# Optimization experiments

Measured on AMD Instinct MI355X. Metric: run time of the kernel, lower is better.

## Reference

```python
import jax, jax.numpy as jnp
import numpy as np

EMBED = 2560
HEADS = 8
HEAD_DIM = EMBED // HEADS

def setup_inputs() -> dict:
    key = jax.random.key(0)
    k1, k2, k3, k4, k5 = jax.random.split(key, 5)
    x = jax.random.normal(k1, (2, 2048, EMBED), dtype=jnp.float32)
    # nn.Linear(embed, 3*embed): weight [3E, E], bias [3E]
    s = 1.0 / np.sqrt(EMBED)
    W_qkv = jax.random.uniform(k2, (3 * EMBED, EMBED), jnp.float32, -s, s)
    b_qkv = jax.random.uniform(k3, (3 * EMBED,), jnp.float32, -s, s)
    W_out = jax.random.uniform(k4, (EMBED, EMBED), jnp.float32, -s, s)
    b_out = jax.random.uniform(k5, (EMBED,), jnp.float32, -s, s)
    return {"x": x, "W_qkv": W_qkv, "b_qkv": b_qkv, "W_out": W_out, "b_out": b_out}

def reference(x, W_qkv, b_qkv, W_out, b_out):
    N, S, E = x.shape
    qkv = jnp.einsum('bse,fe->bsf', x, W_qkv) + b_qkv            # [B,S,3E]
    qkv = qkv.reshape(N, S, 3, HEADS, HEAD_DIM)
    q = jnp.transpose(qkv[:, :, 0], (0, 2, 1, 3))                 # [B,H,S,D]
    k = jnp.transpose(qkv[:, :, 1], (0, 2, 1, 3))
    v = jnp.transpose(qkv[:, :, 2], (0, 2, 1, 3))
    scale = jnp.sqrt(jnp.float32(HEAD_DIM))
    attn = jnp.einsum('bhqd,bhkd->bhqk', q, k) / scale            # [B,H,S,S]
    attn = jax.nn.softmax(attn, axis=-1)
    out = jnp.einsum('bhqk,bhkd->bhqd', attn, v)                  # [B,H,S,D]
    out = jnp.transpose(out, (0, 2, 1, 3)).reshape(N, S, E)
    return jnp.einsum('bse,fe->bsf', out, W_out) + b_out
```

## Files before the change

### kernel.cpp

```cpp
#include <hip/hip_runtime.h>

#define EMBED 2560
#define HEADS 8
#define HDIM  320
#define BATCH 2
#define SEQ   2048
#define MTOT  (BATCH*SEQ)
#define FTOT  (3*EMBED)

using bf = __bf16;
typedef __bf16 bf16x8 __attribute__((ext_vector_type(8)));
typedef float  f32x4  __attribute__((ext_vector_type(4)));
typedef short  s16x8  __attribute__((ext_vector_type(8)));
typedef float  f32x4v __attribute__((ext_vector_type(4)));

__device__ __forceinline__ void gl_lds16(const bf* g, bf* l) {
    __builtin_amdgcn_global_load_lds(
        (const __attribute__((address_space(1))) void*)g,
        (__attribute__((address_space(3))) void*)l,
        16, 0, 0);
}

__global__ void cvt_bf16(const float* __restrict__ in, bf* __restrict__ out, int n) {
    int i = (blockIdx.x*blockDim.x + threadIdx.x)*8;
    if (i >= n) return;
    f32x4v a = *reinterpret_cast<const f32x4v*>(in + i);
    f32x4v b = *reinterpret_cast<const f32x4v*>(in + i + 4);
    bf16x8 r;
    r[0]=(bf)a[0]; r[1]=(bf)a[1]; r[2]=(bf)a[2]; r[3]=(bf)a[3];
    r[4]=(bf)b[0]; r[5]=(bf)b[1]; r[6]=(bf)b[2]; r[7]=(bf)b[3];
    *reinterpret_cast<bf16x8*>(out + i) = r;
}

template<bool OUTBF>
__global__ void gemm_bt(const bf* __restrict__ A, const bf* __restrict__ B,
                        const float* __restrict__ bias, void* __restrict__ Cp,
                        int M, int N, int K) {
    __shared__ bf As[128*32];
    __shared__ bf Bs[128*32];
    const int tid = threadIdx.x, lane = tid & 63, wid = tid >> 6;
    const int wr = wid >> 1, wc = wid & 1;
    const int m0 = blockIdx.y*128, n0 = blockIdx.x*128;
    const int l15 = lane & 15, l4 = lane >> 4;
    f32x4 acc[4][4] = {};

    for (int k0 = 0; k0 < K; k0 += 32) {
        #pragma unroll
        for (int j = 0; j < 2; ++j) {
            int ch  = wid*128 + j*64 + lane;
            int row = ch >> 2, col = (ch & 3)*8;
            gl_lds16(A + (size_t)(m0 + row)*K + k0 + col, As + (wid*128 + j*64)*8);
            gl_lds16(B + (size_t)(n0 + row)*K + k0 + col, Bs + (wid*128 + j*64)*8);
        }
        __syncthreads();
        bf16x8 af[4], bfr[4];
        #pragma unroll
        for (int m = 0; m < 4; ++m)
            af[m] = *reinterpret_cast<const bf16x8*>(&As[(wr*64 + m*16 + l15)*32 + l4*8]);
        #pragma unroll
        for (int n = 0; n < 4; ++n)
            bfr[n] = *reinterpret_cast<const bf16x8*>(&Bs[(wc*64 + n*16 + l15)*32 + l4*8]);
        #pragma unroll
        for (int m = 0; m < 4; ++m)
            #pragma unroll
            for (int n = 0; n < 4; ++n)
                acc[m][n] = __builtin_amdgcn_mfma_f32_16x16x32_bf16(af[m], bfr[n], acc[m][n], 0, 0, 0);
        __syncthreads();
    }
    #pragma unroll
    for (int m = 0; m < 4; ++m) {
        #pragma unroll
        for (int n = 0; n < 4; ++n) {
            int col_g = n0 + wc*64 + n*16 + l15;
            float bv = bias[col_g];
            #pragma unroll
            for (int r = 0; r < 4; ++r) {
                int row_g = m0 + wr*64 + m*16 + l4*4 + r;
                float v = acc[m][n][r] + bv;
                if (OUTBF) ((bf*)Cp)[(size_t)row_g*N + col_g] = (bf)v;
                else       ((float*)Cp)[(size_t)row_g*N + col_g] = v;
            }
        }
    }
}

__global__ void repack_vt(const bf* __restrict__ qkv, bf* __restrict__ vt) {
    __shared__ bf tile[64][72];
    const int bh = blockIdx.z, b = bh >> 3, h = bh & 7;
    const int s0 = blockIdx.x*64, d0 = blockIdx.y*64;
    const int t = threadIdx.x;
    #pragma unroll
    for (int p = 0; p < 2; ++p) {
        int sr = (t >> 3) + p*32, ck = t & 7;
        s16x8 v = *reinterpret_cast<const s16x8*>(
            qkv + ((size_t)(b*SEQ + s0 + sr))*FTOT + 2*EMBED + h*HDIM + d0 + ck*8);
        *reinterpret_cast<s16x8*>(&tile[sr][ck*8]) = v;
    }
    __syncthreads();
    #pragma unroll
    for (int p = 0; p < 2; ++p) {
        int dr = (t >> 3) + p*32, ck = t & 7;
        bf16x8 r;
        #pragma unroll
        for (int j = 0; j < 8; ++j) r[j] = tile[ck*8 + j][dr];
        *reinterpret_cast<bf16x8*>(vt + ((size_t)bh*HDIM + d0 + dr)*SEQ + s0 + ck*8) = r;
    }
}

__global__ __launch_bounds__(512, 2)
void attn_fwd(const bf* __restrict__ qkv, const bf* __restrict__ vt, bf* __restrict__ aout) {
    __shared__ bf Kls[2][32*320];
    __shared__ bf Vls[2][320*32];
    __shared__ bf Ps[8][16][40];
    const int bh = blockIdx.y, b = bh >> 3, h = bh & 7;
    const int tid = threadIdx.x, lane = tid & 63, wid = tid >> 6;
    const int qw = blockIdx.x*128 + wid*16;
    const int l15 = lane & 15, l4 = lane >> 4;
    const float scale = 0.05590169944f;

    const bf* gsrc[5];
    int ldsoff[5];
    size_t step;
    if (wid < 4) {
        step = (size_t)32*FTOT;
        #pragma unroll
        for (int i = 0; i < 5; ++i) {
            int g = wid*5 + i;
            int q = g*64 + lane;
            int r = q/40, cl = q - r*40;
            int cg = cl ^ (r & 7);
            gsrc[i] = qkv + (size_t)(b*SEQ + r)*FTOT + EMBED + h*HDIM + cg*8;
            ldsoff[i] = g*512;
        }
    } else {
        step = 32;
        #pragma unroll
        for (int i = 0; i < 5; ++i) {
            int g = wid*5 + i - 20;
            int q = g*64 + lane;
            int row = q >> 2, cl = q & 3;
            int cg = cl ^ ((row >> 1) & 3);
            gsrc[i] = vt + (size_t)bh*HDIM*SEQ + (size_t)row*SEQ + cg*8;
            ldsoff[i] = g*512;
        }
    }

    bf16x8 qf[10];
    const bf* qbase = qkv + ((size_t)(b*SEQ + qw + l15))*FTOT + h*HDIM + l4*8;
    #pragma unroll
    for (int d = 0; d < 10; ++d) qf[d] = *reinterpret_cast<const bf16x8*>(qbase + d*32);

    f32x4 o[20] = {};
    float mrow[4], lsum[4];
    #pragma unroll
    for (int r = 0; r < 4; ++r) { mrow[r] = -1e30f; lsum[r] = 0.f; }

    const int r7  = l15 & 7;
    const int vsw = (l4 ^ ((l15 >> 1) & 3))*8;

    {
        bf* lb = (wid < 4) ? &Kls[0][0] : &Vls[0][0];
        #pragma unroll
        for (int i = 0; i < 5; ++i) { gl_lds16(gsrc[i], lb + ldsoff[i]); gsrc[i] += step; }
    }
    __syncthreads();

    for (int kt = 0; kt < SEQ/32; ++kt) {
        const int bb = kt & 1;
        if (kt + 1 < SEQ/32) {
            bf* lb = (wid < 4) ? &Kls[bb^1][0] : &Vls[bb^1][0];
            #pragma unroll
            for (int i = 0; i < 5; ++i) { gl_lds16(gsrc[i], lb + ldsoff[i]); gsrc[i] += step; }
        }
        const bf* Kb = &Kls[bb][0];
        const bf* Vb = &Vls[bb][0];

        f32x4 sc[2] = {};
        #pragma unroll
        for (int kb = 0; kb < 2; ++kb) {
            const int Rbase = (kb*16 + l15)*320;
            #pragma unroll
            for (int d = 0; d < 10; ++d) {
                int c = (d*4 + l4) ^ r7;
                bf16x8 kf = *reinterpret_cast<const bf16x8*>(&Kb[Rbase + c*8]);
                sc[kb] = __builtin_amdgcn_mfma_f32_16x16x32_bf16(qf[d], kf, sc[kb], 0, 0, 0);
            }
        }

        float tmax[4];
        bool need = false;
        #pragma unroll
        for (int r = 0; r < 4; ++r) {
            float v = fmaxf(sc[0][r], sc[1][r])*scale;
            v = fmaxf(v, __shfl_xor(v, 1));
            v = fmaxf(v, __shfl_xor(v, 2));
            v = fmaxf(v, __shfl_xor(v, 4));
            v = fmaxf(v, __shfl_xor(v, 8));
            tmax[r] = v;
            need = need || (v > mrow[r] + 8.f);
        }
        if (__any(need)) {
            float alpha[4];
            #pragma unroll
            for (int r = 0; r < 4; ++r) {
                float nm = fmaxf(mrow[r], tmax[r]);
                alpha[r] = __expf(mrow[r] - nm);
                mrow[r] = nm;
                lsum[r] *= alpha[r];
            }
            #pragma unroll
            for (int c = 0; c < 20; ++c)
                #pragma unroll
                for (int r = 0; r < 4; ++r) o[c][r] *= alpha[r];
        }

        float ps[2][4];
        #pragma unroll
        for (int r = 0; r < 4; ++r) {
            float p0 = __expf(sc[0][r]*scale - mrow[r]);
            float p1 = __expf(sc[1][r]*scale - mrow[r]);
            ps[0][r] = p0; ps[1][r] = p1;
            lsum[r] += p0 + p1;
        }

        #pragma unroll
        for (int kb = 0; kb < 2; ++kb)
            #pragma unroll
            for (int r = 0; r < 4; ++r)
                Ps[wid][l4*4 + r][kb*16 + l15] = (bf)ps[kb][r];

        bf16x8 pf = *reinterpret_cast<const bf16x8*>(&Ps[wid][l15][l4*8]);
        #pragma unroll
        for (int c = 0; c < 20; ++c) {
            bf16x8 vf = *reinterpret_cast<const bf16x8*>(&Vb[(c*16 + l15)*32 + vsw]);
            o[c] = __builtin_amdgcn_mfma_f32_16x16x32_bf16(pf, vf, o[c], 0, 0, 0);
        }
        __syncthreads();
    }

    float inv[4];
    #pragma unroll
    for (int r = 0; r < 4; ++r) {
        float s = lsum[r];
        s += __shfl_xor(s, 1);
        s += __shfl_xor(s, 2);
        s += __shfl_xor(s, 4);
        s += __shfl_xor(s, 8);
        inv[r] = 1.f/s;
    }
    #pragma unroll
    for (int c = 0; c < 20; ++c)
        #pragma unroll
        for (int r = 0; r < 4; ++r) {
            size_t idx = ((size_t)(b*SEQ + qw + l4*4 + r))*EMBED + h*HDIM + c*16 + l15;
            aout[idx] = (bf)(o[c][r]*inv[r]);
        }
}

extern "C" void kernel_launch(void* const* d_in, const int* in_sizes, int n_in,
                              void* d_out, int out_size, void* d_ws, size_t ws_size,
                              hipStream_t stream) {
    const float* x    = (const float*)d_in[0];
    const float* Wqkv = (const float*)d_in[1];
    const float* bqkv = (const float*)d_in[2];
    const float* Wout = (const float*)d_in[3];
    const float* bout = (const float*)d_in[4];
    float* out = (float*)d_out;

    char* ws = (char*)d_ws;
    bf* xb    = (bf*)(ws);
    bf* wqkvb = (bf*)(ws + 20971520);
    bf* woutb = (bf*)(ws + 60293120);
    bf* qkvb  = (bf*)(ws + 73400320);
    bf* vtb   = (bf*)(ws + 136314880);
    bf* attnb = xb;

    cvt_bf16<<<5120, 256, 0, stream>>>(x,    xb,    MTOT*EMBED);
    cvt_bf16<<<9600, 256, 0, stream>>>(Wqkv, wqkvb, FTOT*EMBED);
    cvt_bf16<<<3200, 256, 0, stream>>>(Wout, woutb, EMBED*EMBED);

    gemm_bt<true ><<<dim3(FTOT/128,  MTOT/128), 256, 0, stream>>>(xb, wqkvb, bqkv, qkvb, MTOT, FTOT, EMBED);
    repack_vt<<<dim3(SEQ/64, HDIM/64, BATCH*HEADS), 256, 0, stream>>>(qkvb, vtb);
    attn_fwd<<<dim3(SEQ/128, BATCH*HEADS), 512, 0, stream>>>(qkvb, vtb, attnb);
    gemm_bt<false><<<dim3(EMBED/128, MTOT/128), 256, 0, stream>>>(attnb, woutb, bout, out, MTOT, EMBED, EMBED);
}
```

Measured before the change: 492.2 us.

## Replace GEMM with 256x256 double-buffered swizzled LDS pipelined kernel

Swaps the simple 128x128, K=32 single-buffered GEMM for a 256x256-tile, K=64 kernel with 8 waves. It double-buffers A/B halves in LDS, XOR-swizzles the LDS layout to avoid bank conflicts, interleaves async global->LDS loads with MFMA phases under s_setprio, and remaps workgroup IDs so neighbouring blocks share data in cache. The goal is higher MFMA utilisation and fewer barrier stalls in both projection GEMMs. It uses much more LDS and many registers, and the out-projection grid shrinks to 160 blocks, which may leave CUs underused.

```diff
diff --git a/kernel.cpp b/kernel.cpp
--- a/kernel.cpp
+++ b/kernel.cpp
@@ -33,54 +33,166 @@
 }
 
 template<bool OUTBF>
-__global__ void gemm_bt(const bf* __restrict__ A, const bf* __restrict__ B,
-                        const float* __restrict__ bias, void* __restrict__ Cp,
-                        int M, int N, int K) {
-    __shared__ bf As[128*32];
-    __shared__ bf Bs[128*32];
+__global__ __launch_bounds__(512, 2)
+void gemm256(const bf* __restrict__ A, const bf* __restrict__ B,
+             const float* __restrict__ bias, void* __restrict__ Cp,
+             int M, int N, int K) {
+    __shared__ __align__(16) bf AsL[2][2][8192];
+    __shared__ __align__(16) bf BsL[2][2][8192];
     const int tid = threadIdx.x, lane = tid & 63, wid = tid >> 6;
-    const int wr = wid >> 1, wc = wid & 1;
-    const int m0 = blockIdx.y*128, n0 = blockIdx.x*128;
+    const int wr = wid >> 2, wc = wid & 3;
     const int l15 = lane & 15, l4 = lane >> 4;
-    f32x4 acc[4][4] = {};
-
-    for (int k0 = 0; k0 < K; k0 += 32) {
-        #pragma unroll
-        for (int j = 0; j < 2; ++j) {
-            int ch  = wid*128 + j*64 + lane;
-            int row = ch >> 2, col = (ch & 3)*8;
-            gl_lds16(A + (size_t)(m0 + row)*K + k0 + col, As + (wid*128 + j*64)*8);
-            gl_lds16(B + (size_t)(n0 + row)*K + k0 + col, Bs + (wid*128 + j*64)*8);
-        }
-        __syncthreads();
-        bf16x8 af[4], bfr[4];
-        #pragma unroll
-        for (int m = 0; m < 4; ++m)
-            af[m] = *reinterpret_cast<const bf16x8*>(&As[(wr*64 + m*16 + l15)*32 + l4*8]);
-        #pragma unroll
-        for (int n = 0; n < 4; ++n)
-            bfr[n] = *reinterpret_cast<const bf16x8*>(&Bs[(wc*64 + n*16 + l15)*32 + l4*8]);
-        #pragma unroll
-        for (int m = 0; m < 4; ++m)
-            #pragma unroll
-            for (int n = 0; n < 4; ++n)
-                acc[m][n] = __builtin_amdgcn_mfma_f32_16x16x32_bf16(af[m], bfr[n], acc[m][n], 0, 0, 0);
-        __syncthreads();
-    }
-    #pragma unroll
-    for (int m = 0; m < 4; ++m) {
-        #pragma unroll
-        for (int n = 0; n < 4; ++n) {
-            int col_g = n0 + wc*64 + n*16 + l15;
-            float bv = bias[col_g];
-            #pragma unroll
-            for (int r = 0; r < 4; ++r) {
-                int row_g = m0 + wr*64 + m*16 + l4*4 + r;
-                float v = acc[m][n][r] + bv;
-                if (OUTBF) ((bf*)Cp)[(size_t)row_g*N + col_g] = (bf)v;
-                else       ((float*)Cp)[(size_t)row_g*N + col_g] = v;
-            }
-        }
+
+    const int nwg = gridDim.x*gridDim.y;
+    int bid = blockIdx.y*gridDim.x + blockIdx.x;
+    if ((nwg & 7) == 0) bid = (bid & 7)*(nwg >> 3) + (bid >> 3);
+    const int m0 = (bid / gridDim.x)*256, n0 = (bid % gridDim.x)*256;
+    const int NT = K >> 6;
+
+    unsigned aOff[2];
+    #pragma unroll
+    for (int j = 0; j < 2; ++j) {
+        int q = (wid*2 + j)*64 + lane;
+        int r = q >> 3, cs = q & 7;
+        int csrc = ((((cs >> 1) ^ (r & 3)) << 1) | (cs & 1));
+        aOff[j] = (unsigned)r*K + csrc*8;
+    }
+    const bf* Ap = A + (size_t)m0*K;
+    const bf* Bp = B + (size_t)n0*K;
+
+    auto stA = [&](int bb, int h, int kt) {
+        bf* d = &AsL[bb][h][wid*1024];
+        const bf* s = Ap + (size_t)h*128*K + (size_t)kt*64;
+        gl_lds16(s + aOff[0], d);
+        gl_lds16(s + aOff[1], d + 512);
+    };
+    auto stB = [&](int bb, int h, int kt) {
+        bf* d = &BsL[bb][h][wid*1024];
+        const bf* s = Bp + (size_t)h*128*K + (size_t)kt*64;
+        gl_lds16(s + aOff[0], d);
+        gl_lds16(s + aOff[1], d + 512);
+    };
+
+    f32x4 acc[8][4] = {};
+    bf16x8 aR[4][2], bR0[2][2], bR1[2][2];
+
+    stB(0,0,0); stB(0,1,0); stA(0,0,0); stA(0,1,0); stB(1,0,1); stB(1,1,1);
+    asm volatile("s_waitcnt vmcnt(4)" ::: "memory");
+    __builtin_amdgcn_s_barrier();
+
+    const int brow0 = (wc & 1)*64;
+    for (int kt = 0; kt < NT; ++kt) {
+        const int bb = kt & 1;
+        const bf* Ab = &AsL[bb][wr][0];
+        const bf* Bb = &BsL[bb][wc >> 1][0];
+
+        #pragma unroll
+        for (int mi = 0; mi < 4; ++mi)
+            #pragma unroll
+            for (int kk = 0; kk < 2; ++kk) {
+                int r = mi*16 + l15;
+                int g = kk*2 + (l4 >> 1);
+                aR[mi][kk] = *reinterpret_cast<const bf16x8*>(&Ab[r*64 + ((g^(r&3))*16) + (l4&1)*8]);
+            }
+        #pragma unroll
+        for (int ni = 0; ni < 2; ++ni)
+            #pragma unroll
+            for (int kk = 0; kk < 2; ++kk) {
+                int r = brow0 + ni*16 + l15;
+                int g = kk*2 + (l4 >> 1);
+                bR0[ni][kk] = *reinterpret_cast<const bf16x8*>(&Bb[r*64 + ((g^(r&3))*16) + (l4&1)*8]);
+            }
+        if (kt + 1 < NT) stA(bb^1, 0, kt+1);
+        __builtin_amdgcn_s_barrier();
+        asm volatile("s_waitcnt lgkmcnt(0)" ::: "memory");
+        __builtin_amdgcn_sched_barrier(0);
+        __builtin_amdgcn_s_setprio(1);
+        #pragma unroll
+        for (int mi = 0; mi < 4; ++mi)
+            #pragma unroll
+            for (int ni = 0; ni < 2; ++ni)
+                #pragma unroll
+                for (int kk = 0; kk < 2; ++kk)
+                    acc[mi][ni] = __builtin_amdgcn_mfma_f32_16x16x32_bf16(aR[mi][kk], bR0[ni][kk], acc[mi][ni], 0, 0, 0);
+        __builtin_amdgcn_s_setprio(0);
+        __builtin_amdgcn_s_barrier();
+
+        #pragma unroll
+        for (int ni = 0; ni < 2; ++ni)
+            #pragma unroll
+            for (int kk = 0; kk < 2; ++kk) {
+                int r = brow0 + 32 + ni*16 + l15;
+                int g = kk*2 + (l4 >> 1);
+                bR1[ni][kk] = *reinterpret_cast<const bf16x8*>(&Bb[r*64 + ((g^(r&3))*16) + (l4&1)*8]);
+            }
+        if (kt + 1 < NT) stA(bb^1, 1, kt+1);
+        __builtin_amdgcn_s_barrier();
+        asm volatile("s_waitcnt lgkmcnt(0)" ::: "memory");
+        __builtin_amdgcn_sched_barrier(0);
+        __builtin_amdgcn_s_setprio(1);
+        #pragma unroll
+        for (int mi = 0; mi < 4; ++mi)
+            #pragma unroll
+            for (int ni = 0; ni < 2; ++ni)
+                #pragma unroll
+                for (int kk = 0; kk < 2; ++kk)
+                    acc[mi][2+ni] = __builtin_amdgcn_mfma_f32_16x16x32_bf16(aR[mi][kk], bR1[ni][kk], acc[mi][2+ni], 0, 0, 0);
+        __builtin_amdgcn_s_setprio(0);
+        __builtin_amdgcn_s_barrier();
+
+        #pragma unroll
+        for (int mi = 0; mi < 4; ++mi)
+            #pragma unroll
+            for (int kk = 0; kk < 2; ++kk) {
+                int r = 64 + mi*16 + l15;
+                int g = kk*2 + (l4 >> 1);
+                aR[mi][kk] = *reinterpret_cast<const bf16x8*>(&Ab[r*64 + ((g^(r&3))*16) + (l4&1)*8]);
+            }
+        if (kt + 2 < NT) stB(bb, 0, kt+2);
+        __builtin_amdgcn_s_barrier();
+        asm volatile("s_waitcnt lgkmcnt(0)" ::: "memory");
+        __builtin_amdgcn_sched_barrier(0);
+        __builtin_amdgcn_s_setprio(1);
+        #pragma unroll
+        for (int mi = 0; mi < 4; ++mi)
+            #pragma unroll
+            for (int ni = 0; ni < 2; ++ni)
+                #pragma unroll
+                for (int kk = 0; kk < 2; ++kk)
+                    acc[4+mi][2+ni] = __builtin_amdgcn_mfma_f32_16x16x32_bf16(aR[mi][kk], bR1[ni][kk], acc[4+mi][2+ni], 0, 0, 0);
+        __builtin_amdgcn_s_setprio(0);
+        __builtin_amdgcn_s_barrier();
+
+        if (kt + 2 < NT) stB(bb, 1, kt+2);
+        if (kt >= NT-2) asm volatile("s_waitcnt vmcnt(0)" ::: "memory");
+        else            asm volatile("s_waitcnt vmcnt(4)" ::: "memory");
+        __builtin_amdgcn_s_barrier();
+        __builtin_amdgcn_s_setprio(1);
+        #pragma unroll
+        for (int mi = 0; mi < 4; ++mi)
+            #pragma unroll
+            for (int ni = 0; ni < 2; ++ni)
+                #pragma unroll
+                for (int kk = 0; kk < 2; ++kk)
+                    acc[4+mi][ni] = __builtin_amdgcn_mfma_f32_16x16x32_bf16(aR[mi][kk], bR0[ni][kk], acc[4+mi][ni], 0, 0, 0);
+        __builtin_amdgcn_s_setprio(0);
+        __builtin_amdgcn_s_barrier();
+    }
+
+    const int cr0 = m0 + wr*128, cc0 = n0 + wc*64;
+    #pragma unroll
+    for (int NI = 0; NI < 4; ++NI) {
+        int colg = cc0 + NI*16 + l15;
+        float bv = bias[colg];
+        #pragma unroll
+        for (int MI = 0; MI < 8; ++MI)
+            #pragma unroll
+            for (int rr = 0; rr < 4; ++rr) {
+                int rowg = cr0 + MI*16 + l4*4 + rr;
+                float v = acc[MI][NI][rr] + bv;
+                if (OUTBF) ((bf*)Cp)[(size_t)rowg*N + colg] = (bf)v;
+                else       ((float*)Cp)[(size_t)rowg*N + colg] = v;
+            }
     }
 }
 
@@ -279,8 +391,8 @@
     cvt_bf16<<<9600, 256, 0, stream>>>(Wqkv, wqkvb, FTOT*EMBED);
     cvt_bf16<<<3200, 256, 0, stream>>>(Wout, woutb, EMBED*EMBED);
 
-    gemm_bt<true ><<<dim3(FTOT/128,  MTOT/128), 256, 0, stream>>>(xb, wqkvb, bqkv, qkvb, MTOT, FTOT, EMBED);
+    gemm256<true ><<<dim3(FTOT/256,  MTOT/256), 512, 0, stream>>>(xb, wqkvb, bqkv, qkvb, MTOT, FTOT, EMBED);
     repack_vt<<<dim3(SEQ/64, HDIM/64, BATCH*HEADS), 256, 0, stream>>>(qkvb, vtb);
     attn_fwd<<<dim3(SEQ/128, BATCH*HEADS), 512, 0, stream>>>(qkvb, vtb, attnb);
-    gemm_bt<false><<<dim3(EMBED/128, MTOT/128), 256, 0, stream>>>(attnb, woutb, bout, out, MTOT, EMBED, EMBED);
-}
+    gemm256<false><<<dim3(EMBED/256, MTOT/256), 512, 0, stream>>>(attnb, woutb, bout, out, MTOT, EMBED, EMBED);
+}
```

Result: faster. 435.2 us (-11.6%).
